# Kernel tuning notes

Measured on AMD Instinct MI355X. Metric: run time of the kernel, lower is better.

## Reference

```python
import jax, jax.numpy as jnp
import numpy as np

IMG = 32            # feature-map side == image_size
B, HC = 8, 3        # batch, hint channels
C, NH, L = 256, 8, 8  # model_channels, nhead, num_encoder_layers
DFF = 1025
HIN = IMG * 8       # hint resolution (three stride-2 convs => /8)
NEIGH = (7, 7)
CONV_SHAPES = [(16, HC), (16, 16), (32, 16), (32, 32), (96, 32), (96, 96), (256, 96), (C, 256)]
STRIDES = [1, 1, 2, 1, 2, 1, 2, 1]


def setup_inputs() -> dict:
    key = jax.random.key(0)
    ks = jax.random.split(key, 32)
    inp = {"hint": jax.random.normal(ks[0], (B, HC, HIN, HIN), jnp.float32)}
    for i, (co, ci) in enumerate(CONV_SHAPES):
        inp[f"conv_w{i}"] = jax.random.normal(ks[1 + i], (co, ci, 3, 3), jnp.float32) * 0.05
    base = 9
    def p(shape, j):
        return jax.random.normal(ks[base + j], (L,) + shape, jnp.float32) * 0.02
    inp["in_proj_w"] = p((3 * C, C), 0)
    inp["in_proj_b"] = p((3 * C,), 1)
    inp["out_w"] = p((C, C), 2)
    inp["out_b"] = p((C,), 3)
    inp["lin1_w"] = p((DFF, C), 4)
    inp["lin1_b"] = p((DFF,), 5)
    inp["lin2_w"] = p((C, DFF), 6)
    inp["lin2_b"] = p((C,), 7)
    inp["ln1_w"] = jnp.ones((L, C), jnp.float32)
    inp["ln1_b"] = jnp.zeros((L, C), jnp.float32)
    inp["ln2_w"] = jnp.ones((L, C), jnp.float32)
    inp["ln2_b"] = jnp.zeros((L, C), jnp.float32)
    return inp


def _conv(x, w, s):
    # torch Conv2d(k=3, padding=1, stride=s, bias=False)
    return jax.lax.conv_general_dilated(x, w, (s, s), [(1, 1), (1, 1)],
                                        dimension_numbers=("NCHW", "OIHW", "NCHW"))


def _sine_pos(h, w, c):
    # DETR/UniAD PositionEmbeddingSine (normalize=False, temperature=1e4) -> (h*w, c)
    npf = c // 2
    y = jnp.broadcast_to(jnp.arange(1, h + 1, dtype=jnp.float32)[:, None], (h, w))
    x = jnp.broadcast_to(jnp.arange(1, w + 1, dtype=jnp.float32)[None, :], (h, w))
    dim_t = 10000.0 ** (2.0 * (jnp.arange(npf, dtype=jnp.float32) // 2) / npf)
    px = x[..., None] / dim_t
    py = y[..., None] / dim_t
    px = jnp.stack([jnp.sin(px[..., 0::2]), jnp.cos(px[..., 1::2])], -1).reshape(h, w, npf)
    py = jnp.stack([jnp.sin(py[..., 0::2]), jnp.cos(py[..., 1::2])], -1).reshape(h, w, npf)
    return jnp.concatenate([py, px], -1).reshape(h * w, c)


def _neigh_mask(h, w, hm, wm):
    # vectorized version of generate_mask: 0 inside the hm x wm neighborhood, -inf outside
    ih = jnp.arange(h)
    iw = jnp.arange(w)
    dh = jnp.abs(ih[:, None] - ih[None, :]) <= hm // 2   # (h, h)
    dw = jnp.abs(iw[:, None] - iw[None, :]) <= wm // 2   # (w, w)
    allowed = (dh[:, None, :, None] & dw[None, :, None, :]).reshape(h * w, h * w)
    return jnp.where(allowed, 0.0, -1e9).astype(jnp.float32)


def _ln(x, g, b):
    mu = x.mean(-1, keepdims=True)
    v = ((x - mu) ** 2).mean(-1, keepdims=True)
    return (x - mu) / jnp.sqrt(v + 1e-5) * g + b


def _forward(hint, conv_ws, params):
    x = hint
    for i, (w, s) in enumerate(zip(conv_ws, STRIDES)):
        x = _conv(x, w, s)
        if i < len(conv_ws) - 1:
            x = jax.nn.silu(x)
    b, c, h, w = x.shape
    src = x.reshape(b, c, h * w).transpose(0, 2, 1)          # (B, N, C), N h-major
    pos = _sine_pos(h, w, c)[None]                           # (1, N, C)
    mask = _neigh_mask(h, w, *NEIGH)                         # (N, N)
    dh = c // NH
    scale = 1.0 / np.sqrt(dh).astype(np.float32)

    def layer(s, p):
        ipw, ipb, ow, ob, l1w, l1b, l2w, l2b, g1, b1, g2, b2 = p
        qk_in = s + pos
        q = (qk_in @ ipw[:c].T + ipb[:c]).reshape(b, -1, NH, dh)
        k = (qk_in @ ipw[c:2 * c].T + ipb[c:2 * c]).reshape(b, -1, NH, dh)
        v = (s @ ipw[2 * c:].T + ipb[2 * c:]).reshape(b, -1, NH, dh)
        sc = jnp.einsum('bnhd,bmhd->bhnm', q, k) * scale + mask
        a = jax.nn.softmax(sc, -1)
        ctx = jnp.einsum('bhnm,bmhd->bnhd', a, v).reshape(b, -1, c)
        s = _ln(s + ctx @ ow.T + ob, g1, b1)                 # post-norm
        ff = jax.nn.relu(s @ l1w.T + l1b) @ l2w.T + l2b      # dropout inactive (eval)
        return _ln(s + ff, g2, b2), None

    src, _ = jax.lax.scan(layer, src, params)
    return src.transpose(0, 2, 1).reshape(b, c, h, w)        # '(h w) b c -> b c h w'


def reference(hint, conv_w0, conv_w1, conv_w2, conv_w3, conv_w4, conv_w5, conv_w6, conv_w7,
              in_proj_w, in_proj_b, out_w, out_b, lin1_w, lin1_b, lin2_w, lin2_b,
              ln1_w, ln1_b, ln2_w, ln2_b):
    conv_ws = (conv_w0, conv_w1, conv_w2, conv_w3, conv_w4, conv_w5, conv_w6, conv_w7)
    params = (in_proj_w, in_proj_b, out_w, out_b, lin1_w, lin1_b, lin2_w, lin2_b,
              ln1_w, ln1_b, ln2_w, ln2_b)
    return _forward(hint, conv_ws, params)
```

## Files before the change

kernel.cpp:

```cpp
#include <hip/hip_runtime.h>
#include <hip/hip_bf16.h>


typedef __bf16 bf16x8 __attribute__((ext_vector_type(8)));
typedef float f32x4 __attribute__((ext_vector_type(4)));
typedef unsigned short us8v __attribute__((ext_vector_type(8)));

__device__ __forceinline__ unsigned short f2bf(float f) {
  unsigned int u = __float_as_uint(f);
  unsigned int r = (u + 0x7fffu + ((u >> 16) & 1u)) >> 16;
  return (unsigned short)r;
}
__device__ __forceinline__ float bf2f(unsigned short h) {
  return __uint_as_float(((unsigned int)h) << 16);
}

#define GLD16(src, dst)                                                        \
  __builtin_amdgcn_global_load_lds(                                            \
      (const __attribute__((address_space(1))) unsigned int*)(src),            \
      (__attribute__((address_space(3))) unsigned int*)(dst), 16, 0, 0)

template<int BM, int BN, int NT, int MODE, int LNF = 0, int KTC = 0>
__global__ __launch_bounds__(NT) void k_gemm(
    const unsigned short* __restrict__ A, int lda,
    const unsigned short* __restrict__ Bw, int ldb,
    const float* __restrict__ bias, const float* __restrict__ posadd,
    float* __restrict__ C, unsigned short* __restrict__ Cb, int ldc,
    int K, int Nstore, int act, int omode, long long zsB, long long zsC,
    const unsigned short* __restrict__ zpage, int Ci, int Hi, int stride, int lw,
    int divm, int divs, const float* __restrict__ lng, const float* __restrict__ lnb)
{
  constexpr int NW = NT / 64;
  constexpr int NWN = (NT == 512) ? 4 : ((BN >= 128) ? 2 : 1);
  constexpr int NWM = NW / NWN;
  constexpr int WM = BM / NWM, WN = BN / NWN;
  constexpr int MF = WM / 16, NF = WN / 16;
  constexpr int AIS = (BM * 8) / NT;
  constexpr int BIS = (BN * 8) / NT;
  __shared__ unsigned short lA[2][BM * 64];
  __shared__ unsigned short lB[2][BN * 64];
  int tid = threadIdx.x, lane = tid & 63, wid = tid >> 6;
  int bm = blockIdx.x * BM, bn = blockIdx.y * BN;
  const unsigned short* Bz = Bw + (size_t)blockIdx.z * zsB;

  int j = (lane & 7) ^ (lane >> 3);
  int e8 = (j & 3) << 3;
  int halfl = j >> 2;

  size_t arow[AIS], brow[BIS];
  int hb[AIS], wb[AIS];
  size_t ab[AIS];
#pragma unroll
  for (int i = 0; i < AIS; ++i) {
    int rr = (wid + i * NW) * 8 + (lane >> 3);
    if constexpr (MODE == 0) {
      arow[i] = (size_t)(bm + rr) * lda + (j << 3);
    } else {
      int pos = bm + rr;
      int b = pos >> (2 * lw);
      int rem = pos & ((1 << (2 * lw)) - 1);
      int ho = rem >> lw, wo = rem & ((1 << lw) - 1);
      hb[i] = ho * stride - 1;
      wb[i] = wo * stride - 1;
      ab[i] = (size_t)b * Hi * Hi * Ci;
    }
  }
#pragma unroll
  for (int i = 0; i < BIS; ++i)
    brow[i] = (size_t)(bn + (wid + i * NW) * 8 + (lane >> 3)) * ldb + (j << 3);

  auto stage = [&](int buf, int kt) {
    if constexpr (MODE == 1) {
      int s0 = kt * 2, s1 = s0 + 1;
      int t0 = (s0 * divm) >> divs, t1 = (s1 * divm) >> divs;
      int cipw = Ci >> 5;
      int cc0 = (s0 - t0 * cipw) << 5, cc1 = (s1 - t1 * cipw) << 5;
      int kh0 = (t0 * 171) >> 9, kw0 = t0 - kh0 * 3;
      int kh1 = (t1 * 171) >> 9, kw1 = t1 - kh1 * 3;
      int kh = halfl ? kh1 : kh0;
      int kw = halfl ? kw1 : kw0;
      int cco = halfl ? cc1 : cc0;
      bool tv = (halfl ? t1 : t0) < 9;
#pragma unroll
      for (int i = 0; i < AIS; ++i) {
        int hi = hb[i] + kh, wi = wb[i] + kw;
        const unsigned short* ap =
            (tv && (unsigned)hi < (unsigned)Hi && (unsigned)wi < (unsigned)Hi)
                ? (A + ab[i] + (size_t)(hi * Hi + wi) * Ci + cco + e8)
                : zpage;
        GLD16(ap, &lA[buf][(wid + i * NW) * 512]);
      }
    } else {
#pragma unroll
      for (int i = 0; i < AIS; ++i)
        GLD16(A + arow[i] + kt * 64, &lA[buf][(wid + i * NW) * 512]);
    }
#pragma unroll
    for (int i = 0; i < BIS; ++i)
      GLD16(Bz + brow[i] + kt * 64, &lB[buf][(wid + i * NW) * 512]);
  };

  f32x4 acc[MF][NF];
#pragma unroll
  for (int m = 0; m < MF; ++m)
#pragma unroll
    for (int n = 0; n < NF; ++n)
#pragma unroll
      for (int q = 0; q < 4; ++q) acc[m][n][q] = 0.f;

  int wn = wid % NWN, wm = wid / NWN;
  int r0 = wm * WM + (lane & 15);
  int c0 = wn * WN + (lane & 15);
  int sl0 = (((lane >> 4)) ^ (lane & 7)) << 3;
  int sl1 = (((lane >> 4) + 4) ^ (lane & 7)) << 3;
  const int nkt = (KTC > 0) ? KTC : (K >> 6);
  int cur = 0;
  stage(0, 0);
#pragma unroll
  for (int kt = 0; kt < nkt; ++kt) {
    if (kt + 1 < nkt) {
      stage(cur ^ 1, kt + 1);
      asm volatile("s_waitcnt vmcnt(%0)" : : "n"(AIS + BIS) : "memory");
    } else {
      asm volatile("s_waitcnt vmcnt(0)" : : : "memory");
    }
    __builtin_amdgcn_s_barrier();
    asm volatile("" ::: "memory");
    bf16x8 a0[MF], a1[MF], b0[NF], b1[NF];
#pragma unroll
    for (int m = 0; m < MF; ++m) {
      a0[m] = *(const bf16x8*)&lA[cur][(r0 + m * 16) * 64 + sl0];
      a1[m] = *(const bf16x8*)&lA[cur][(r0 + m * 16) * 64 + sl1];
    }
#pragma unroll
    for (int n = 0; n < NF; ++n) {
      b0[n] = *(const bf16x8*)&lB[cur][(c0 + n * 16) * 64 + sl0];
      b1[n] = *(const bf16x8*)&lB[cur][(c0 + n * 16) * 64 + sl1];
    }
#pragma unroll
    for (int m = 0; m < MF; ++m)
#pragma unroll
      for (int n = 0; n < NF; ++n)
        acc[m][n] = __builtin_amdgcn_mfma_f32_16x16x32_bf16(a0[m], b0[n], acc[m][n], 0, 0, 0);
#pragma unroll
    for (int m = 0; m < MF; ++m)
#pragma unroll
      for (int n = 0; n < NF; ++n)
        acc[m][n] = __builtin_amdgcn_mfma_f32_16x16x32_bf16(a1[m], b1[n], acc[m][n], 0, 0, 0);
    asm volatile("" ::: "memory");
    __builtin_amdgcn_s_barrier();
    cur ^= 1;
  }

  int colb = bn + wn * WN + (lane & 15);
  int rowb = bm + wm * WM + ((lane >> 4) << 2);
  float* Cz = C ? C + (size_t)blockIdx.z * zsC : nullptr;
  unsigned short* Cbz = Cb ? Cb + (size_t)blockIdx.z * zsC : nullptr;
#pragma unroll
  for (int n = 0; n < NF; ++n) {
    int col = colb + n * 16;
    if (col >= Nstore) continue;
    float bs = bias ? bias[col] : 0.f;
#pragma unroll
    for (int m = 0; m < MF; ++m) {
#pragma unroll
      for (int q = 0; q < 4; ++q) {
        int row = rowb + m * 16 + q;
        float v = acc[m][n][q] + bs;
        if (posadd && col < 512) v += posadd[((row & 1023) << 9) + col];
        if (act == 1) v = fmaxf(v, 0.f);
        else if (act == 2) v = v / (1.f + __expf(-v));
        size_t off = (size_t)row * ldc + col;
        if (omode == 0) Cz[off] = v;
        else if (omode == 1) Cbz[off] = f2bf(v);
        else { Cz[off] = v; Cbz[off] = f2bf(v); }
      }
    }
  }
}

__global__ __launch_bounds__(256) void k_mlp(
    const unsigned short* __restrict__ ctx, const unsigned short* __restrict__ wo,
    const float* __restrict__ ob,
    const unsigned short* __restrict__ w1, const float* __restrict__ b1,
    const unsigned short* __restrict__ w2, const float* __restrict__ b2,
    float* __restrict__ src, unsigned short* __restrict__ sbo,
    const float* __restrict__ g1, const float* __restrict__ lb1,
    const float* __restrict__ g2, const float* __restrict__ lb2)
{
  __shared__ unsigned short aT[4][32 * 64];
  __shared__ unsigned short lB[2][256 * 64];
  __shared__ unsigned short ffl[32][1160];
  __shared__ float red[2][32][2];
  int tid = threadIdx.x, lane = tid & 63, wid = tid >> 6;
  int bm = blockIdx.x << 5;
  int j = (lane & 7) ^ (lane >> 3);
  int rsrc = lane >> 3;

  {
    int rr = wid * 8 + rsrc;
    const unsigned short* ap = ctx + (size_t)(bm + rr) * 256 + (j << 3);
#pragma unroll
    for (int kt = 0; kt < 4; ++kt)
      GLD16(ap + kt * 64, &aT[kt][wid * 512]);
  }
  size_t brow256[8], brow1152[8];
#pragma unroll
  for (int i = 0; i < 8; ++i) {
    int rr = (wid + i * 4) * 8 + rsrc;
    brow256[i]  = (size_t)rr * 256 + (j << 3);
    brow1152[i] = (size_t)rr * 1152 + (j << 3);
  }
  auto stageWo = [&](int buf, int kt) {
#pragma unroll
    for (int i = 0; i < 8; ++i)
      GLD16(wo + brow256[i] + kt * 64, &lB[buf][(wid + i * 4) * 512]);
  };
  auto stageB1 = [&](int buf, int s) {
    int ny = s >> 2, kt = s & 3;
#pragma unroll
    for (int i = 0; i < 4; ++i)
      GLD16(w1 + (size_t)ny * 128 * 256 + brow256[i] + kt * 64, &lB[buf][(wid + i * 4) * 512]);
  };
  auto stageB2 = [&](int buf, int kt) {
#pragma unroll
    for (int i = 0; i < 8; ++i)
      GLD16(w2 + brow1152[i] + kt * 64, &lB[buf][(wid + i * 4) * 512]);
  };

  int wn = wid & 1, wm = wid >> 1;
  int r0 = wm * 16 + (lane & 15);
  int sl0 = ((lane >> 4) ^ (lane & 7)) << 3;
  int sl1 = (((lane >> 4) + 4) ^ (lane & 7)) << 3;
  int kqa = (lane >> 4) << 3;
  int c02 = wn * 128 + (lane & 15);
  int rowl = wm * 16 + ((lane >> 4) << 2);

  stageWo(0, 0);
  int cur = 0;
  f32x4 acco[8];
#pragma unroll
  for (int n = 0; n < 8; ++n)
#pragma unroll
    for (int q = 0; q < 4; ++q) acco[n][q] = 0.f;
#pragma unroll
  for (int kt = 0; kt < 4; ++kt) {
    if (kt + 1 < 4) {
      stageWo(cur ^ 1, kt + 1);
      asm volatile("s_waitcnt vmcnt(8)" : : : "memory");
    } else {
      asm volatile("s_waitcnt vmcnt(0)" : : : "memory");
    }
    __builtin_amdgcn_s_barrier();
    asm volatile("" ::: "memory");
    bf16x8 a0 = *(const bf16x8*)&aT[kt][r0 * 64 + sl0];
    bf16x8 a1 = *(const bf16x8*)&aT[kt][r0 * 64 + sl1];
    bf16x8 b0v[8], b1v[8];
#pragma unroll
    for (int n = 0; n < 8; ++n) {
      b0v[n] = *(const bf16x8*)&lB[cur][(c02 + n * 16) * 64 + sl0];
      b1v[n] = *(const bf16x8*)&lB[cur][(c02 + n * 16) * 64 + sl1];
    }
#pragma unroll
    for (int n = 0; n < 8; ++n)
      acco[n] = __builtin_amdgcn_mfma_f32_16x16x32_bf16(a0, b0v[n], acco[n], 0, 0, 0);
#pragma unroll
    for (int n = 0; n < 8; ++n)
      acco[n] = __builtin_amdgcn_mfma_f32_16x16x32_bf16(a1, b1v[n], acco[n], 0, 0, 0);
    asm volatile("" ::: "memory");
    __builtin_amdgcn_s_barrier();
    cur ^= 1;
  }
  stageB1(0, 0);

  float resid[8][4];
  {
    float x[8][4];
    float sums[4] = {0.f, 0.f, 0.f, 0.f}, sqs[4] = {0.f, 0.f, 0.f, 0.f};
#pragma unroll
    for (int n = 0; n < 8; ++n) {
      int col = c02 + n * 16;
      float bs = ob[col];
#pragma unroll
      for (int q = 0; q < 4; ++q) {
        float v = acco[n][q] + bs + src[(size_t)(bm + rowl + q) * 256 + col];
        x[n][q] = v;
        sums[q] += v;
        sqs[q] += v * v;
      }
    }
#pragma unroll
    for (int q = 0; q < 4; ++q) {
      sums[q] += __shfl_xor(sums[q], 1); sqs[q] += __shfl_xor(sqs[q], 1);
      sums[q] += __shfl_xor(sums[q], 2); sqs[q] += __shfl_xor(sqs[q], 2);
      sums[q] += __shfl_xor(sums[q], 4); sqs[q] += __shfl_xor(sqs[q], 4);
      sums[q] += __shfl_xor(sums[q], 8); sqs[q] += __shfl_xor(sqs[q], 8);
    }
    if ((lane & 15) == 0) {
#pragma unroll
      for (int q = 0; q < 4; ++q) {
        red[wn][rowl + q][0] = sums[q];
        red[wn][rowl + q][1] = sqs[q];
      }
    }
    __syncthreads();
#pragma unroll
    for (int q = 0; q < 4; ++q) {
      float ts = sums[q] + red[wn ^ 1][rowl + q][0];
      float tq = sqs[q] + red[wn ^ 1][rowl + q][1];
      float mu = ts * (1.f / 256.f);
      float var = tq * (1.f / 256.f) - mu * mu;
      float rs = rsqrtf(var + 1e-5f);
      int r = rowl + q;
#pragma unroll
      for (int n = 0; n < 8; ++n) {
        int col = c02 + n * 16;
        float o = (x[n][q] - mu) * rs * g1[col] + lb1[col];
        resid[n][q] = o;
        int kt = col >> 6, jj = (col >> 3) & 7, e = col & 7;
        aT[kt][r * 64 + (((jj ^ (r & 7))) << 3) + e] = f2bf(o);
      }
    }
  }
  __syncthreads();

  cur = 0;
  for (int ny = 0; ny < 9; ++ny) {
    f32x4 acc1[4];
#pragma unroll
    for (int n = 0; n < 4; ++n)
#pragma unroll
      for (int q = 0; q < 4; ++q) acc1[n][q] = 0.f;
    int c01 = wn * 64 + (lane & 15);
#pragma unroll
    for (int kt = 0; kt < 4; ++kt) {
      int s = ny * 4 + kt;
      if (s + 1 < 36) {
        stageB1(cur ^ 1, s + 1);
        asm volatile("s_waitcnt vmcnt(4)" : : : "memory");
      } else {
        asm volatile("s_waitcnt vmcnt(0)" : : : "memory");
      }
      __builtin_amdgcn_s_barrier();
      asm volatile("" ::: "memory");
      bf16x8 a0 = *(const bf16x8*)&aT[kt][r0 * 64 + sl0];
      bf16x8 a1 = *(const bf16x8*)&aT[kt][r0 * 64 + sl1];
      bf16x8 b0v[4], b1v[4];
#pragma unroll
      for (int n = 0; n < 4; ++n) {
        b0v[n] = *(const bf16x8*)&lB[cur][(c01 + n * 16) * 64 + sl0];
        b1v[n] = *(const bf16x8*)&lB[cur][(c01 + n * 16) * 64 + sl1];
      }
#pragma unroll
      for (int n = 0; n < 4; ++n)
        acc1[n] = __builtin_amdgcn_mfma_f32_16x16x32_bf16(a0, b0v[n], acc1[n], 0, 0, 0);
#pragma unroll
      for (int n = 0; n < 4; ++n)
        acc1[n] = __builtin_amdgcn_mfma_f32_16x16x32_bf16(a1, b1v[n], acc1[n], 0, 0, 0);
      asm volatile("" ::: "memory");
      __builtin_amdgcn_s_barrier();
      cur ^= 1;
    }
    int rowe = wm * 16 + ((lane >> 4) << 2);
#pragma unroll
    for (int n = 0; n < 4; ++n) {
      int col = ny * 128 + c01 + n * 16;
      float bs = b1[col];
#pragma unroll
      for (int q = 0; q < 4; ++q)
        ffl[rowe + q][col] = f2bf(fmaxf(acc1[n][q] + bs, 0.f));
    }
  }

  stageB2(0, 0);
  __syncthreads();
  cur = 0;
  f32x4 acc[8];
#pragma unroll
  for (int n = 0; n < 8; ++n)
#pragma unroll
    for (int q = 0; q < 4; ++q) acc[n][q] = 0.f;
#pragma unroll
  for (int kt = 0; kt < 18; ++kt) {
    if (kt + 1 < 18) {
      stageB2(cur ^ 1, kt + 1);
      asm volatile("s_waitcnt vmcnt(8)" : : : "memory");
    } else {
      asm volatile("s_waitcnt vmcnt(0)" : : : "memory");
    }
    __builtin_amdgcn_s_barrier();
    asm volatile("" ::: "memory");
    bf16x8 a0 = *(const bf16x8*)&ffl[r0][kt * 64 + kqa];
    bf16x8 a1 = *(const bf16x8*)&ffl[r0][kt * 64 + 32 + kqa];
    bf16x8 b0v[8], b1v[8];
#pragma unroll
    for (int n = 0; n < 8; ++n) {
      b0v[n] = *(const bf16x8*)&lB[cur][(c02 + n * 16) * 64 + sl0];
      b1v[n] = *(const bf16x8*)&lB[cur][(c02 + n * 16) * 64 + sl1];
    }
#pragma unroll
    for (int n = 0; n < 8; ++n)
      acc[n] = __builtin_amdgcn_mfma_f32_16x16x32_bf16(a0, b0v[n], acc[n], 0, 0, 0);
#pragma unroll
    for (int n = 0; n < 8; ++n)
      acc[n] = __builtin_amdgcn_mfma_f32_16x16x32_bf16(a1, b1v[n], acc[n], 0, 0, 0);
    asm volatile("" ::: "memory");
    __builtin_amdgcn_s_barrier();
    cur ^= 1;
  }

  float x[8][4];
  float sums[4] = {0.f, 0.f, 0.f, 0.f}, sqs[4] = {0.f, 0.f, 0.f, 0.f};
#pragma unroll
  for (int n = 0; n < 8; ++n) {
    int col = c02 + n * 16;
    float bs = b2[col];
#pragma unroll
    for (int q = 0; q < 4; ++q) {
      float v = acc[n][q] + bs + resid[n][q];
      x[n][q] = v;
      sums[q] += v;
      sqs[q] += v * v;
    }
  }
#pragma unroll
  for (int q = 0; q < 4; ++q) {
    sums[q] += __shfl_xor(sums[q], 1); sqs[q] += __shfl_xor(sqs[q], 1);
    sums[q] += __shfl_xor(sums[q], 2); sqs[q] += __shfl_xor(sqs[q], 2);
    sums[q] += __shfl_xor(sums[q], 4); sqs[q] += __shfl_xor(sqs[q], 4);
    sums[q] += __shfl_xor(sums[q], 8); sqs[q] += __shfl_xor(sqs[q], 8);
  }
  if ((lane & 15) == 0) {
#pragma unroll
    for (int q = 0; q < 4; ++q) {
      red[wn][rowl + q][0] = sums[q];
      red[wn][rowl + q][1] = sqs[q];
    }
  }
  __syncthreads();
#pragma unroll
  for (int q = 0; q < 4; ++q) {
    float ts = sums[q] + red[wn ^ 1][rowl + q][0];
    float tq = sqs[q] + red[wn ^ 1][rowl + q][1];
    float mu = ts * (1.f / 256.f);
    float var = tq * (1.f / 256.f) - mu * mu;
    float rs = rsqrtf(var + 1e-5f);
    int row = bm + rowl + q;
#pragma unroll
    for (int n = 0; n < 8; ++n) {
      int col = c02 + n * 16;
      float o = (x[n][q] - mu) * rs * g2[col] + lb2[col];
      src[(size_t)row * 256 + col] = o;
      sbo[(size_t)row * 256 + col] = f2bf(o);
    }
  }
}

__global__ __launch_bounds__(256) void k_conv0(
    const float* __restrict__ x, const float* __restrict__ w,
    unsigned short* __restrict__ y)
{
  __shared__ float ws[16][28];
  int tid = threadIdx.x;
  for (int u = tid; u < 432; u += 256) {
    int co = u / 27, k = u - co * 27;
    int t = k / 3, ci = k - t * 3;
    ws[co][k] = w[((size_t)co * 3 + ci) * 9 + t];
  }
  __syncthreads();
  int h = blockIdx.x, b = blockIdx.y, wo = tid;
  float xin[3][3][3];
#pragma unroll
  for (int ci = 0; ci < 3; ++ci)
#pragma unroll
    for (int kh = 0; kh < 3; ++kh) {
      int hi = h + kh - 1;
#pragma unroll
      for (int kw = 0; kw < 3; ++kw) {
        int wi = wo + kw - 1;
        xin[ci][kh][kw] = ((unsigned)hi < 256u && (unsigned)wi < 256u)
            ? x[(((size_t)b * 3 + ci) << 16) + (hi << 8) + wi] : 0.f;
      }
    }
  float acc[16] = {};
#pragma unroll
  for (int t = 0; t < 9; ++t) {
    const int kh = t / 3, kw = t % 3;
#pragma unroll
    for (int ci = 0; ci < 3; ++ci) {
      float xv = xin[ci][kh][kw];
#pragma unroll
      for (int co = 0; co < 16; ++co)
        acc[co] = fmaf(xv, ws[co][t * 3 + ci], acc[co]);
    }
  }
  us8v o0, o1, zv;
#pragma unroll
  for (int q = 0; q < 8; ++q) {
    float v0 = acc[q];     v0 = v0 / (1.f + __expf(-v0)); o0[q] = f2bf(v0);
    float v1 = acc[q + 8]; v1 = v1 / (1.f + __expf(-v1)); o1[q] = f2bf(v1);
    zv[q] = 0;
  }
  unsigned short* yp = y + ((((size_t)b << 16) + (h << 8) + wo) << 5);
  *(us8v*)(yp) = o0; *(us8v*)(yp + 8) = o1;
  *(us8v*)(yp + 16) = zv; *(us8v*)(yp + 24) = zv;
}

template<int S>
__global__ __launch_bounds__(256) void k_conv_direct(
    const unsigned short* __restrict__ x, const unsigned short* __restrict__ wp,
    int ldw, unsigned short* __restrict__ y, int Hi, int Ho, int Wo, int lwt)
{
  constexpr int HR = 7 * S + 3;
  constexpr int HC = 15 * S + 3;
  constexpr int HP = HR * HC;
  __shared__ unsigned short xs[HP * 40];
  __shared__ unsigned short wsh[32 * 312];
  int tid = threadIdx.x, lane = tid & 63, wv = tid >> 6;
  int b = blockIdx.y;
  int tr = blockIdx.x >> lwt, tc = blockIdx.x & ((1 << lwt) - 1);
  int hi0 = tr * 8 * S - 1, wi0 = tc * 16 * S - 1;

  for (int u = tid; u < HP * 8; u += 256) {
    int pix = u >> 3, part = u & 7;
    int hr = pix / HC, hcc = pix - hr * HC;
    int hi = hi0 + hr, wi = wi0 + hcc;
    ushort4 v = {0, 0, 0, 0};
    if ((unsigned)hi < (unsigned)Hi && (unsigned)wi < (unsigned)Hi)
      v = *(const ushort4*)(x + ((size_t)(b * Hi + hi) * Hi + wi) * 32 + part * 4);
    *(ushort4*)(&xs[pix * 40 + part * 4]) = v;
  }
  for (int u = tid; u < 2304; u += 256) {
    int co = u / 72, kk = (u - co * 72) * 4;
    *(ushort4*)(&wsh[co * 312 + kk]) = *(const ushort4*)(wp + (size_t)co * ldw + kk);
  }
  __syncthreads();

  int cL = lane & 15, kq = (lane >> 4) << 3;
  f32x4 acc[2][2];
#pragma unroll
  for (int m = 0; m < 2; ++m)
#pragma unroll
    for (int n = 0; n < 2; ++n)
#pragma unroll
      for (int q = 0; q < 4; ++q) acc[m][n][q] = 0.f;

#pragma unroll
  for (int tap = 0; tap < 9; ++tap) {
    const int kh = tap / 3, kw = tap % 3;
    bf16x8 af[2], bfr[2];
#pragma unroll
    for (int m = 0; m < 2; ++m) {
      int hr = (wv * 2 + m) * S + kh;
      int hc = cL * S + kw;
      af[m] = *(const bf16x8*)&xs[(hr * HC + hc) * 40 + kq];
    }
#pragma unroll
    for (int n = 0; n < 2; ++n)
      bfr[n] = *(const bf16x8*)&wsh[(cL + n * 16) * 312 + tap * 32 + kq];
#pragma unroll
    for (int m = 0; m < 2; ++m)
#pragma unroll
      for (int n = 0; n < 2; ++n)
        acc[m][n] = __builtin_amdgcn_mfma_f32_16x16x32_bf16(af[m], bfr[n], acc[m][n], 0, 0, 0);
  }

  int wo0 = tc * 16 + ((lane >> 4) << 2);
#pragma unroll
  for (int m = 0; m < 2; ++m) {
    int ho = tr * 8 + wv * 2 + m;
#pragma unroll
    for (int n = 0; n < 2; ++n) {
      int co = cL + n * 16;
#pragma unroll
      for (int q = 0; q < 4; ++q) {
        float v = acc[m][n][q];
        v = v / (1.f + __expf(-v));
        y[((size_t)(b * Ho + ho) * Wo + wo0 + q) * 32 + co] = f2bf(v);
      }
    }
  }
}

struct WP8 { const float* w[8]; unsigned short* q[8]; };
__global__ __launch_bounds__(256) void k_wperm_all(WP8 p)
{
  const int CoPs[8]  = {128, 32, 32, 32, 128, 128, 256, 256};
  const int CiRs[8]  = {3, 16, 16, 32, 32, 96, 96, 256};
  const int CiPs[8]  = {3, 32, 32, 32, 32, 96, 96, 256};
  const int Kpads[8] = {64, 288, 288, 288, 320, 896, 896, 2304};
  const int Cos[8]   = {16, 16, 32, 32, 96, 96, 256, 256};
  int i = blockIdx.y + 1;
  const float* w = p.w[i];
  unsigned short* wp = p.q[i];
  int Kpad = Kpads[i], CiP = CiPs[i], CiR = CiRs[i], Co = Cos[i];
  int total = CoPs[i] * Kpad;
  for (int idx = blockIdx.x * 256 + threadIdx.x; idx < total; idx += gridDim.x * 256) {
    int co = idx / Kpad, k = idx - co * Kpad;
    int t = k / CiP, ci = k - t * CiP;
    float v = 0.f;
    if (co < Co && t < 9 && ci < CiR) v = w[((size_t)co * CiR + ci) * 9 + t];
    wp[idx] = f2bf(v);
  }
}

struct PrepArgs {
  const float *ipw, *outw, *l1w, *l2w, *l1b;
  unsigned short *wqkvb, *outwb, *l1wb, *l2wb, *posb;
  float *l1bp;
};
__global__ __launch_bounds__(256) void k_prep(PrepArgs a)
{
  int seg = blockIdx.y;
  int idx0 = blockIdx.x * 256 + threadIdx.x;
  int stride = gridDim.x * 256;
  if (seg == 0) {
    for (int i = idx0; i < 8 * 768 * 256; i += stride) a.wqkvb[i] = f2bf(a.ipw[i]);
  } else if (seg == 1) {
    for (int i = idx0; i < 8 * 256 * 256; i += stride) a.outwb[i] = f2bf(a.outw[i]);
  } else if (seg == 2) {
    for (int i = idx0; i < 8 * 1152 * 256; i += stride) {
      int l = i / (1152 * 256), r = (i >> 8) % 1152, c = i & 255;
      float v = (r < 1025) ? a.l1w[((size_t)l * 1025 + r) * 256 + c] : 0.f;
      a.l1wb[i] = f2bf(v);
    }
  } else if (seg == 3) {
    for (int i = idx0; i < 8 * 256 * 1152; i += stride) {
      int l = i / (256 * 1152), rc = i % (256 * 1152), r = rc / 1152, c = rc - (rc / 1152) * 1152;
      float v = (c < 1025) ? a.l2w[((size_t)l * 256 + r) * 1025 + c] : 0.f;
      a.l2wb[i] = f2bf(v);
    }
  } else if (seg == 4) {
    for (int i = idx0; i < 8 * 1152; i += stride) {
      int l = i / 1152, c = i - l * 1152;
      a.l1bp[i] = (c < 1025) ? a.l1b[l * 1025 + c] : 0.f;
    }
  } else {
    for (int i = idx0; i < 1024 * 256; i += stride) {
      int n = i >> 8, c = i & 255;
      int ih = n >> 5, iw = n & 31;
      float coord = (c < 128) ? (float)(ih + 1) : (float)(iw + 1);
      int cc = c & 127;
      float e = (float)((cc >> 1) << 1) * (1.f / 128.f);
      float t = coord / powf(10000.f, e);
      a.posb[i] = f2bf((cc & 1) ? cosf(t) : sinf(t));
    }
  }
}

__global__ __launch_bounds__(256) void k_attn(
    const unsigned short* __restrict__ qkv, unsigned short* __restrict__ ctx)
{
  __shared__ unsigned short k_ldsu[848 * 8];
  __shared__ unsigned short v_lds[848 * 8];
  __shared__ float p_lds[64 * 50];
  int bx = blockIdx.x;
  int b = bx >> 4, tile = bx & 15;
  int th8 = ((tile >> 2) << 3), tw8 = ((tile & 3) << 3);
  int g = blockIdx.y;
  int tid = threadIdx.x, lane = tid & 63, wid = tid >> 6;
  int h0e = max(th8 - 3, 0), h1e = min(th8 + 10, 31);
  int w0e = max(tw8 - 3, 0), w1e = min(tw8 + 10, 31);
  int nh = h1e - h0e + 1, nw = w1e - w0e + 1;
  int nkeys = nh * nw, nslots = nkeys * 4;
  unsigned int magic = (65536u + (unsigned)nw - 1u) / (unsigned)nw;
  size_t qbase = (size_t)((unsigned)b << 10) * 768;

#pragma unroll
  for (int i = 0; i < 4; ++i) {
    int base = i * 256 + wid * 64;
    if (base < 784) {
      int s = min(base + lane, nslots - 1);
      int uidx = s >> 2, chunk = s & 3;
      int hh = (int)(((unsigned)uidx * magic) >> 16);
      int ww = uidx - hh * nw;
      hh += h0e; ww += w0e;
      const unsigned short* rp = qkv + qbase + (size_t)((hh << 5) + ww) * 768 + (g << 5) + chunk * 8;
      GLD16(rp + 256, &k_ldsu[base * 8]);
      GLD16(rp + 512, &v_lds[base * 8]);
    }
  }
  __syncthreads();

  int q = tid >> 2, dq = tid & 3;
  int qh = th8 + (q >> 3), qw = tw8 + (q & 7);
  const float scale = 0.17677669529663687f;
  const unsigned short* qp = qkv + qbase + (size_t)((qh << 5) + qw) * 768 + (g << 5) + dq * 8;
  us8v uq = *(const us8v*)qp;
  float qr[8];
#pragma unroll
  for (int t = 0; t < 8; ++t) qr[t] = bf2f(uq[t]) * scale;

  int rbase[7], cofs[7];
  bool rval[7], cval[7];
#pragma unroll
  for (int d = 0; d < 7; ++d) {
    int mh = qh - 3 + d;
    rval[d] = (unsigned)mh < 32u;
    rbase[d] = (mh - h0e) * nw;
    int mw = qw - 3 + d;
    cval[d] = (unsigned)mw < 32u;
    cofs[d] = mw - w0e;
  }

  float m = -1e30f;
#pragma unroll
  for (int kk = 0; kk < 49; ++kk) {
    const int d7 = kk / 7, r7 = kk % 7;
    bool valid = rval[d7] && cval[r7];
    int uidx = valid ? (rbase[d7] + cofs[r7]) : 0;
    us8v uk = *(const us8v*)&k_ldsu[uidx * 32 + dq * 8];
    float d = 0.f;
#pragma unroll
    for (int t = 0; t < 8; ++t) d = fmaf(qr[t], bf2f(uk[t]), d);
    d += __shfl_xor(d, 1);
    d += __shfl_xor(d, 2);
    float s_kk = valid ? d : -1e30f;
    m = fmaxf(m, s_kk);
    if (dq == (kk & 3)) p_lds[q * 50 + kk] = s_kk;
  }
  float sum = 0.f;
  for (int kk = dq; kk < 49; kk += 4) {
    float e = __expf(p_lds[q * 50 + kk] - m);
    p_lds[q * 50 + kk] = e;
    sum += e;
  }
  sum += __shfl_xor(sum, 1);
  sum += __shfl_xor(sum, 2);
  float inv = 1.f / sum;

  float acc[8] = {};
#pragma unroll
  for (int kk = 0; kk < 49; ++kk) {
    const int d7 = kk / 7, r7 = kk % 7;
    int uidx = (rval[d7] && cval[r7]) ? (rbase[d7] + cofs[r7]) : 0;
    float pb = p_lds[q * 50 + kk];
    us8v uv = *(const us8v*)&v_lds[uidx * 32 + dq * 8];
#pragma unroll
    for (int t = 0; t < 8; ++t) acc[t] = fmaf(pb, bf2f(uv[t]), acc[t]);
  }
  unsigned short* op = ctx + ((size_t)((b << 10) + (qh << 5) + qw) << 8) + (g << 5) + dq * 8;
  us8v out;
#pragma unroll
  for (int t = 0; t < 8; ++t) out[t] = f2bf(acc[t] * inv);
  *(us8v*)op = out;
}

__global__ void k_nxc_to_cxn(const float* __restrict__ x, float* __restrict__ y)
{
  __shared__ float t[32][33];
  int b = blockIdx.z;
  int c0 = blockIdx.x * 32, n0 = blockIdx.y * 32;
  int tx = threadIdx.x, ty = threadIdx.y;
  t[ty][tx] = x[((size_t)(b * 1024 + n0 + ty)) * 256 + c0 + tx];
  __syncthreads();
  y[((size_t)(b * 256 + c0 + ty)) * 1024 + n0 + tx] = t[tx][ty];
}

extern "C" void kernel_launch(void* const* d_in, const int* in_sizes, int n_in,
                              void* d_out, int out_size, void* d_ws, size_t ws_size,
                              hipStream_t stream)
{
  const float* hint = (const float*)d_in[0];
  const float* cw[8];
  for (int i = 0; i < 8; ++i) cw[i] = (const float*)d_in[1 + i];
  const float* ipw  = (const float*)d_in[9];
  const float* ipb  = (const float*)d_in[10];
  const float* outw = (const float*)d_in[11];
  const float* outb = (const float*)d_in[12];
  const float* l1w  = (const float*)d_in[13];
  const float* l1b  = (const float*)d_in[14];
  const float* l2w  = (const float*)d_in[15];
  const float* l2b  = (const float*)d_in[16];
  const float* g1   = (const float*)d_in[17];
  const float* b1   = (const float*)d_in[18];
  const float* g2   = (const float*)d_in[19];
  const float* b2   = (const float*)d_in[20];

  float* ws = (float*)d_ws;
  size_t off = 0;
  float* bufA = ws + off; off += 8388608;
  float* bufB = ws + off; off += 8388608;
  float* src  = ws + off; off += 2097152;
  unsigned short* srcb = (unsigned short*)(ws + off); off += 1048576;
  unsigned short* posb = (unsigned short*)(ws + off); off += 131072;
  float* posqk = ws + off; off += 4194304;
  unsigned short* wqkvb = (unsigned short*)(ws + off); off += 786432;
  unsigned short* outwb = (unsigned short*)(ws + off); off += 262144;
  unsigned short* l1wb  = (unsigned short*)(ws + off); off += 1179648;
  unsigned short* l2wb  = (unsigned short*)(ws + off); off += 1179648;
  float* l1bp = ws + off; off += 9216;
  unsigned short* cwp[8];
  const int CoPs[8]  = {128, 32, 32, 32, 128, 128, 256, 256};
  const int Kpads[8] = {64, 288, 288, 288, 320, 896, 896, 2304};
  for (int i = 0; i < 8; ++i) { cwp[i] = (unsigned short*)(ws + off); off += ((size_t)CoPs[i] * Kpads[i] + 1) / 2; }
  unsigned short* zpage = (unsigned short*)(ws + off); off += 64;

  hipMemsetAsync(zpage, 0, 256, stream);

  PrepArgs pa;
  pa.ipw = ipw; pa.outw = outw; pa.l1w = l1w; pa.l2w = l2w; pa.l1b = l1b;
  pa.wqkvb = wqkvb; pa.outwb = outwb; pa.l1wb = l1wb; pa.l2wb = l2wb;
  pa.posb = posb; pa.l1bp = l1bp;
  k_prep<<<dim3(256, 6), 256, 0, stream>>>(pa);
  WP8 wpargs;
  for (int i = 0; i < 8; ++i) { wpargs.w[i] = cw[i]; wpargs.q[i] = cwp[i]; }
  k_wperm_all<<<dim3(64, 7), 256, 0, stream>>>(wpargs);

  unsigned short* bufAu = (unsigned short*)bufA;
  unsigned short* bufBu = (unsigned short*)bufB;

#define GEMM_TAIL nullptr, 0, 0, 0, 0, 0, 0, nullptr, nullptr
  k_conv0<<<dim3(256, 8), 256, 0, stream>>>(hint, cw[0], bufAu);
  k_conv_direct<1><<<dim3(512, 8), 256, 0, stream>>>(bufAu, cwp[1], 288, bufBu, 256, 256, 256, 4);
  k_conv_direct<2><<<dim3(128, 8), 256, 0, stream>>>(bufBu, cwp[2], 288, bufAu, 256, 128, 128, 3);
  k_conv_direct<1><<<dim3(128, 8), 256, 0, stream>>>(bufAu, cwp[3], 288, bufBu, 128, 128, 128, 3);
  k_gemm<128, 128, 512, 1, 0, 5><<<dim3(256, 1), 512, 0, stream>>>(
      bufBu, 0, cwp[4], 320, nullptr, nullptr, nullptr, bufAu, 96, 320, 96, 2, 1,
      0, 0, zpage, 32, 128, 2, 6, 1, 0, nullptr, nullptr);
  k_gemm<128, 128, 512, 1, 0, 14><<<dim3(256, 1), 512, 0, stream>>>(
      bufAu, 0, cwp[5], 896, nullptr, nullptr, nullptr, bufBu, 96, 896, 96, 2, 1,
      0, 0, zpage, 96, 64, 1, 6, 171, 9, nullptr, nullptr);
  k_gemm<64, 128, 512, 1, 0, 14><<<dim3(128, 2), 512, 0, stream>>>(
      bufBu, 0, cwp[6], 896, nullptr, nullptr, nullptr, bufAu, 256, 896, 256, 2, 1,
      0, 0, zpage, 96, 64, 2, 5, 171, 9, nullptr, nullptr);
  k_gemm<64, 128, 512, 1><<<dim3(128, 2), 512, 0, stream>>>(
      bufAu, 0, cwp[7], 2304, nullptr, nullptr, src, srcb, 256, 2304, 256, 0, 2,
      0, 0, zpage, 256, 32, 1, 5, 1, 3, nullptr, nullptr);

  k_gemm<64, 128, 512, 0, 0, 4><<<dim3(16, 4, 8), 512, 0, stream>>>(
      posb, 256, wqkvb, 256, nullptr, nullptr, posqk, nullptr, 512, 256, 512, 0, 0,
      196608LL, 524288LL, GEMM_TAIL);

  unsigned short* qkvb = bufAu;
  unsigned short* ctx  = (unsigned short*)(bufA + 3145728);

  for (int l = 0; l < 8; ++l) {
    const unsigned short* wqkv_l = wqkvb + (size_t)l * 768 * 256;
    const float* ipb_l  = ipb  + (size_t)l * 768;
    const unsigned short* outw_l = outwb + (size_t)l * 256 * 256;
    const float* outb_l = outb + (size_t)l * 256;
    const unsigned short* l1w_l = l1wb + (size_t)l * 1152 * 256;
    const float* l1b_l  = l1bp + (size_t)l * 1152;
    const unsigned short* l2w_l = l2wb + (size_t)l * 256 * 1152;
    const float* l2b_l  = l2b  + (size_t)l * 256;
    const float* posqk_l = posqk + (size_t)l * 524288;
    const float* g1_l = g1 + l * 256; const float* b1_l = b1 + l * 256;
    const float* g2_l = g2 + l * 256; const float* b2_l = b2 + l * 256;

    k_gemm<64, 128, 512, 0, 0, 4><<<dim3(128, 6), 512, 0, stream>>>(
        srcb, 256, wqkv_l, 256, ipb_l, posqk_l, nullptr, qkvb, 768, 256, 768, 0, 1,
        0, 0, GEMM_TAIL);
    k_attn<<<dim3(128, 8), 256, 0, stream>>>(qkvb, ctx);
    k_mlp<<<dim3(256), 256, 0, stream>>>(
        ctx, outw_l, outb_l, l1w_l, l1b_l, l2w_l, l2b_l,
        src, srcb, g1_l, b1_l, g2_l, b2_l);
  }

  k_nxc_to_cxn<<<dim3(8, 32, 8), dim3(32, 32), 0, stream>>>(src, (float*)d_out);
}
```

Measured before the change: 849.8 us.

## Unify MLP weight staging into a 4-deep continuous prefetch pipeline across GEMMs

```diff
diff --git a/kernel.cpp b/kernel.cpp
--- a/kernel.cpp
+++ b/kernel.cpp
@@ -189,102 +189,90 @@
     const float* __restrict__ g2, const float* __restrict__ lb2)
 {
   __shared__ unsigned short aT[4][32 * 64];
-  __shared__ unsigned short lB[2][256 * 64];
+  __shared__ unsigned short lB[4][128 * 64];
   __shared__ unsigned short ffl[32][1160];
   __shared__ float red[2][32][2];
   int tid = threadIdx.x, lane = tid & 63, wid = tid >> 6;
   int bm = blockIdx.x << 5;
-  int j = (lane & 7) ^ (lane >> 3);
   int rsrc = lane >> 3;
+  int jj8 = ((lane & 7) ^ rsrc) << 3;
 
   {
     int rr = wid * 8 + rsrc;
-    const unsigned short* ap = ctx + (size_t)(bm + rr) * 256 + (j << 3);
+    const unsigned short* ap = ctx + (size_t)(bm + rr) * 256 + jj8;
 #pragma unroll
     for (int kt = 0; kt < 4; ++kt)
       GLD16(ap + kt * 64, &aT[kt][wid * 512]);
   }
-  size_t brow256[8], brow1152[8];
-#pragma unroll
-  for (int i = 0; i < 8; ++i) {
-    int rr = (wid + i * 4) * 8 + rsrc;
-    brow256[i]  = (size_t)rr * 256 + (j << 3);
-    brow1152[i] = (size_t)rr * 1152 + (j << 3);
-  }
-  auto stageWo = [&](int buf, int kt) {
-#pragma unroll
-    for (int i = 0; i < 8; ++i)
-      GLD16(wo + brow256[i] + kt * 64, &lB[buf][(wid + i * 4) * 512]);
+
+  auto issue = [&](int s) {
+    const unsigned short* base;
+    int ld, coloff, row0;
+    if (s < 8)       { base = wo; ld = 256;  coloff = (s >> 1) * 64; row0 = (s & 1) * 128; }
+    else if (s < 44) { int t = s - 8;  base = w1; ld = 256;  coloff = (t & 3) * 64; row0 = (t >> 2) * 128; }
+    else             { int t = s - 44; base = w2; ld = 1152; coloff = (t >> 1) * 64; row0 = (t & 1) * 128; }
+    int buf = s & 3;
+#pragma unroll
+    for (int i = 0; i < 4; ++i) {
+      int rr = row0 + (wid + i * 4) * 8 + rsrc;
+      GLD16(base + (size_t)rr * ld + coloff + jj8, &lB[buf][(wid + i * 4) * 512]);
+    }
   };
-  auto stageB1 = [&](int buf, int s) {
-    int ny = s >> 2, kt = s & 3;
-#pragma unroll
-    for (int i = 0; i < 4; ++i)
-      GLD16(w1 + (size_t)ny * 128 * 256 + brow256[i] + kt * 64, &lB[buf][(wid + i * 4) * 512]);
-  };
-  auto stageB2 = [&](int buf, int kt) {
-#pragma unroll
-    for (int i = 0; i < 8; ++i)
-      GLD16(w2 + brow1152[i] + kt * 64, &lB[buf][(wid + i * 4) * 512]);
-  };
+  issue(0); issue(1); issue(2); issue(3);
 
   int wn = wid & 1, wm = wid >> 1;
   int r0 = wm * 16 + (lane & 15);
   int sl0 = ((lane >> 4) ^ (lane & 7)) << 3;
   int sl1 = (((lane >> 4) + 4) ^ (lane & 7)) << 3;
   int kqa = (lane >> 4) << 3;
-  int c02 = wn * 128 + (lane & 15);
+  int cbase = wn * 16 + (lane & 15);
   int rowl = wm * 16 + ((lane >> 4) << 2);
 
-  stageWo(0, 0);
-  int cur = 0;
   f32x4 acco[8];
 #pragma unroll
-  for (int n = 0; n < 8; ++n)
-#pragma unroll
-    for (int q = 0; q < 4; ++q) acco[n][q] = 0.f;
-#pragma unroll
-  for (int kt = 0; kt < 4; ++kt) {
-    if (kt + 1 < 4) {
-      stageWo(cur ^ 1, kt + 1);
-      asm volatile("s_waitcnt vmcnt(8)" : : : "memory");
-    } else {
-      asm volatile("s_waitcnt vmcnt(0)" : : : "memory");
-    }
+  for (int m = 0; m < 8; ++m)
+#pragma unroll
+    for (int q = 0; q < 4; ++q) acco[m][q] = 0.f;
+#pragma unroll
+  for (int s = 0; s < 8; ++s) {
+    const int kt = s >> 1, rh = s & 1;
+    asm volatile("s_waitcnt vmcnt(12)" ::: "memory");
     __builtin_amdgcn_s_barrier();
     asm volatile("" ::: "memory");
     bf16x8 a0 = *(const bf16x8*)&aT[kt][r0 * 64 + sl0];
     bf16x8 a1 = *(const bf16x8*)&aT[kt][r0 * 64 + sl1];
-    bf16x8 b0v[8], b1v[8];
-#pragma unroll
-    for (int n = 0; n < 8; ++n) {
-      b0v[n] = *(const bf16x8*)&lB[cur][(c02 + n * 16) * 64 + sl0];
-      b1v[n] = *(const bf16x8*)&lB[cur][(c02 + n * 16) * 64 + sl1];
-    }
-#pragma unroll
-    for (int n = 0; n < 8; ++n)
-      acco[n] = __builtin_amdgcn_mfma_f32_16x16x32_bf16(a0, b0v[n], acco[n], 0, 0, 0);
-#pragma unroll
-    for (int n = 0; n < 8; ++n)
-      acco[n] = __builtin_amdgcn_mfma_f32_16x16x32_bf16(a1, b1v[n], acco[n], 0, 0, 0);
+    bf16x8 b0v[4], b1v[4];
+#pragma unroll
+    for (int nn = 0; nn < 4; ++nn) {
+      int rowb = cbase + nn * 32;
+      b0v[nn] = *(const bf16x8*)&lB[s & 3][rowb * 64 + sl0];
+      b1v[nn] = *(const bf16x8*)&lB[s & 3][rowb * 64 + sl1];
+    }
+    __builtin_amdgcn_s_setprio(1);
+#pragma unroll
+    for (int nn = 0; nn < 4; ++nn)
+      acco[rh * 4 + nn] = __builtin_amdgcn_mfma_f32_16x16x32_bf16(a0, b0v[nn], acco[rh * 4 + nn], 0, 0, 0);
+#pragma unroll
+    for (int nn = 0; nn < 4; ++nn)
+      acco[rh * 4 + nn] = __builtin_amdgcn_mfma_f32_16x16x32_bf16(a1, b1v[nn], acco[rh * 4 + nn], 0, 0, 0);
+    __builtin_amdgcn_s_setprio(0);
     asm volatile("" ::: "memory");
     __builtin_amdgcn_s_barrier();
-    cur ^= 1;
-  }
-  stageB1(0, 0);
+    issue(s + 4);
+  }
 
   float resid[8][4];
   {
     float x[8][4];
     float sums[4] = {0.f, 0.f, 0.f, 0.f}, sqs[4] = {0.f, 0.f, 0.f, 0.f};
 #pragma unroll
-    for (int n = 0; n < 8; ++n) {
-      int col = c02 + n * 16;
+    for (int m = 0; m < 8; ++m) {
+      int col = ((m >> 2) << 7) + cbase + ((m & 3) << 5);
       float bs = ob[col];
 #pragma unroll
       for (int q = 0; q < 4; ++q) {
-        float v = acco[n][q] + bs + src[(size_t)(bm + rowl + q) * 256 + col];
-        x[n][q] = v;
+        float v = acco[m][q] + bs + src[(size_t)(bm + rowl + q) * 256 + col];
+        x[m][q] = v;
         sums[q] += v;
         sqs[q] += v * v;
       }
@@ -303,7 +291,9 @@
         red[wn][rowl + q][1] = sqs[q];
       }
     }
-    __syncthreads();
+    asm volatile("s_waitcnt lgkmcnt(0)" ::: "memory");
+    __builtin_amdgcn_s_barrier();
+    asm volatile("" ::: "memory");
 #pragma unroll
     for (int q = 0; q < 4; ++q) {
       float ts = sums[q] + red[wn ^ 1][rowl + q][0];
@@ -313,112 +303,111 @@
       float rs = rsqrtf(var + 1e-5f);
       int r = rowl + q;
 #pragma unroll
-      for (int n = 0; n < 8; ++n) {
-        int col = c02 + n * 16;
-        float o = (x[n][q] - mu) * rs * g1[col] + lb1[col];
-        resid[n][q] = o;
-        int kt = col >> 6, jj = (col >> 3) & 7, e = col & 7;
-        aT[kt][r * 64 + (((jj ^ (r & 7))) << 3) + e] = f2bf(o);
+      for (int m = 0; m < 8; ++m) {
+        int col = ((m >> 2) << 7) + cbase + ((m & 3) << 5);
+        float o = (x[m][q] - mu) * rs * g1[col] + lb1[col];
+        resid[m][q] = o;
+        int kt = col >> 6, jjc = (col >> 3) & 7, e = col & 7;
+        aT[kt][r * 64 + ((jjc ^ (r & 7)) << 3) + e] = f2bf(o);
       }
     }
   }
-  __syncthreads();
-
-  cur = 0;
+  asm volatile("s_waitcnt lgkmcnt(0)" ::: "memory");
+  __builtin_amdgcn_s_barrier();
+  asm volatile("" ::: "memory");
+
   for (int ny = 0; ny < 9; ++ny) {
     f32x4 acc1[4];
 #pragma unroll
-    for (int n = 0; n < 4; ++n)
-#pragma unroll
-      for (int q = 0; q < 4; ++q) acc1[n][q] = 0.f;
-    int c01 = wn * 64 + (lane & 15);
+    for (int nn = 0; nn < 4; ++nn)
+#pragma unroll
+      for (int q = 0; q < 4; ++q) acc1[nn][q] = 0.f;
 #pragma unroll
     for (int kt = 0; kt < 4; ++kt) {
-      int s = ny * 4 + kt;
-      if (s + 1 < 36) {
-        stageB1(cur ^ 1, s + 1);
-        asm volatile("s_waitcnt vmcnt(4)" : : : "memory");
-      } else {
-        asm volatile("s_waitcnt vmcnt(0)" : : : "memory");
-      }
+      int s = 8 + ny * 4 + kt;
+      asm volatile("s_waitcnt vmcnt(12)" ::: "memory");
       __builtin_amdgcn_s_barrier();
       asm volatile("" ::: "memory");
       bf16x8 a0 = *(const bf16x8*)&aT[kt][r0 * 64 + sl0];
       bf16x8 a1 = *(const bf16x8*)&aT[kt][r0 * 64 + sl1];
       bf16x8 b0v[4], b1v[4];
 #pragma unroll
-      for (int n = 0; n < 4; ++n) {
-        b0v[n] = *(const bf16x8*)&lB[cur][(c01 + n * 16) * 64 + sl0];
-        b1v[n] = *(const bf16x8*)&lB[cur][(c01 + n * 16) * 64 + sl1];
+      for (int nn = 0; nn < 4; ++nn) {
+        int rowb = cbase + nn * 32;
+        b0v[nn] = *(const bf16x8*)&lB[s & 3][rowb * 64 + sl0];
+        b1v[nn] = *(const bf16x8*)&lB[s & 3][rowb * 64 + sl1];
       }
-#pragma unroll
-      for (int n = 0; n < 4; ++n)
-        acc1[n] = __builtin_amdgcn_mfma_f32_16x16x32_bf16(a0, b0v[n], acc1[n], 0, 0, 0);
-#pragma unroll
-      for (int n = 0; n < 4; ++n)
-        acc1[n] = __builtin_amdgcn_mfma_f32_16x16x32_bf16(a1, b1v[n], acc1[n], 0, 0, 0);
+      __builtin_amdgcn_s_setprio(1);
+#pragma unroll
+      for (int nn = 0; nn < 4; ++nn)
+        acc1[nn] = __builtin_amdgcn_mfma_f32_16x16x32_bf16(a0, b0v[nn], acc1[nn], 0, 0, 0);
+#pragma unroll
+      for (int nn = 0; nn < 4; ++nn)
+        acc1[nn] = __builtin_amdgcn_mfma_f32_16x16x32_bf16(a1, b1v[nn], acc1[nn], 0, 0, 0);
+      __builtin_amdgcn_s_setprio(0);
       asm volatile("" ::: "memory");
       __builtin_amdgcn_s_barrier();
-      cur ^= 1;
-    }
-    int rowe = wm * 16 + ((lane >> 4) << 2);
-#pragma unroll
-    for (int n = 0; n < 4; ++n) {
-      int col = ny * 128 + c01 + n * 16;
+      issue(s + 4);
+    }
+#pragma unroll
+    for (int nn = 0; nn < 4; ++nn) {
+      int col = ny * 128 + cbase + nn * 32;
       float bs = b1[col];
 #pragma unroll
       for (int q = 0; q < 4; ++q)
-        ffl[rowe + q][col] = f2bf(fmaxf(acc1[n][q] + bs, 0.f));
-    }
-  }
-
-  stageB2(0, 0);
-  __syncthreads();
-  cur = 0;
+        ffl[rowl + q][col] = f2bf(fmaxf(acc1[nn][q] + bs, 0.f));
+    }
+  }
+  asm volatile("s_waitcnt lgkmcnt(0)" ::: "memory");
+
   f32x4 acc[8];
 #pragma unroll
-  for (int n = 0; n < 8; ++n)
-#pragma unroll
-    for (int q = 0; q < 4; ++q) acc[n][q] = 0.f;
-#pragma unroll
+  for (int m = 0; m < 8; ++m)
+#pragma unroll
+    for (int q = 0; q < 4; ++q) acc[m][q] = 0.f;
   for (int kt = 0; kt < 18; ++kt) {
-    if (kt + 1 < 18) {
-      stageB2(cur ^ 1, kt + 1);
-      asm volatile("s_waitcnt vmcnt(8)" : : : "memory");
-    } else {
-      asm volatile("s_waitcnt vmcnt(0)" : : : "memory");
-    }
-    __builtin_amdgcn_s_barrier();
-    asm volatile("" ::: "memory");
-    bf16x8 a0 = *(const bf16x8*)&ffl[r0][kt * 64 + kqa];
-    bf16x8 a1 = *(const bf16x8*)&ffl[r0][kt * 64 + 32 + kqa];
-    bf16x8 b0v[8], b1v[8];
-#pragma unroll
-    for (int n = 0; n < 8; ++n) {
-      b0v[n] = *(const bf16x8*)&lB[cur][(c02 + n * 16) * 64 + sl0];
-      b1v[n] = *(const bf16x8*)&lB[cur][(c02 + n * 16) * 64 + sl1];
-    }
-#pragma unroll
-    for (int n = 0; n < 8; ++n)
-      acc[n] = __builtin_amdgcn_mfma_f32_16x16x32_bf16(a0, b0v[n], acc[n], 0, 0, 0);
-#pragma unroll
-    for (int n = 0; n < 8; ++n)
-      acc[n] = __builtin_amdgcn_mfma_f32_16x16x32_bf16(a1, b1v[n], acc[n], 0, 0, 0);
-    asm volatile("" ::: "memory");
-    __builtin_amdgcn_s_barrier();
-    cur ^= 1;
+#pragma unroll
+    for (int rh = 0; rh < 2; ++rh) {
+      int t = kt * 2 + rh;
+      if (t <= 32) { asm volatile("s_waitcnt vmcnt(12)" ::: "memory"); }
+      else if (t == 33) { asm volatile("s_waitcnt vmcnt(8)" ::: "memory"); }
+      else if (t == 34) { asm volatile("s_waitcnt vmcnt(4)" ::: "memory"); }
+      else { asm volatile("s_waitcnt vmcnt(0)" ::: "memory"); }
+      __builtin_amdgcn_s_barrier();
+      asm volatile("" ::: "memory");
+      bf16x8 a0 = *(const bf16x8*)&ffl[r0][kt * 64 + kqa];
+      bf16x8 a1 = *(const bf16x8*)&ffl[r0][kt * 64 + 32 + kqa];
+      bf16x8 b0v[4], b1v[4];
+#pragma unroll
+      for (int nn = 0; nn < 4; ++nn) {
+        int rowb = cbase + nn * 32;
+        b0v[nn] = *(const bf16x8*)&lB[(44 + t) & 3][rowb * 64 + sl0];
+        b1v[nn] = *(const bf16x8*)&lB[(44 + t) & 3][rowb * 64 + sl1];
+      }
+      __builtin_amdgcn_s_setprio(1);
+#pragma unroll
+      for (int nn = 0; nn < 4; ++nn)
+        acc[rh * 4 + nn] = __builtin_amdgcn_mfma_f32_16x16x32_bf16(a0, b0v[nn], acc[rh * 4 + nn], 0, 0, 0);
+#pragma unroll
+      for (int nn = 0; nn < 4; ++nn)
+        acc[rh * 4 + nn] = __builtin_amdgcn_mfma_f32_16x16x32_bf16(a1, b1v[nn], acc[rh * 4 + nn], 0, 0, 0);
+      __builtin_amdgcn_s_setprio(0);
+      asm volatile("" ::: "memory");
+      __builtin_amdgcn_s_barrier();
+      if (t < 32) issue(48 + t);
+    }
   }
 
   float x[8][4];
   float sums[4] = {0.f, 0.f, 0.f, 0.f}, sqs[4] = {0.f, 0.f, 0.f, 0.f};
 #pragma unroll
-  for (int n = 0; n < 8; ++n) {
-    int col = c02 + n * 16;
+  for (int m = 0; m < 8; ++m) {
+    int col = ((m >> 2) << 7) + cbase + ((m & 3) << 5);
     float bs = b2[col];
 #pragma unroll
     for (int q = 0; q < 4; ++q) {
-      float v = acc[n][q] + bs + resid[n][q];
-      x[n][q] = v;
+      float v = acc[m][q] + bs + resid[m][q];
+      x[m][q] = v;
       sums[q] += v;
       sqs[q] += v * v;
     }
@@ -430,6 +419,7 @@
     sums[q] += __shfl_xor(sums[q], 4); sqs[q] += __shfl_xor(sqs[q], 4);
     sums[q] += __shfl_xor(sums[q], 8); sqs[q] += __shfl_xor(sqs[q], 8);
   }
+  __syncthreads();
   if ((lane & 15) == 0) {
 #pragma unroll
     for (int q = 0; q < 4; ++q) {
@@ -447,9 +437,9 @@
     float rs = rsqrtf(var + 1e-5f);
     int row = bm + rowl + q;
 #pragma unroll
-    for (int n = 0; n < 8; ++n) {
-      int col = c02 + n * 16;
-      float o = (x[n][q] - mu) * rs * g2[col] + lb2[col];
+    for (int m = 0; m < 8; ++m) {
+      int col = ((m >> 2) << 7) + cbase + ((m & 3) << 5);
+      float o = (x[m][q] - mu) * rs * g2[col] + lb2[col];
       src[(size_t)row * 256 + col] = o;
       sbo[(size_t)row * 256 + col] = f2bf(o);
     }
```

Measured after the change: 844.1 us. No clear change (-0.7%).
